# Kernel optimization log

Measured on AMD Instinct MI355X. Metric: run time of the kernel, lower is better.

## Reference

```python
import jax, jax.numpy as jnp
import numpy as np
from jax import lax

K = 3          # dcn kernel size
KK = K * K     # 9 taps
PAD = 1


def _conv(x, w, b, pad):
    y = lax.conv_general_dilated(
        x, w, window_strides=(1, 1), padding=[(pad, pad), (pad, pad)],
        dimension_numbers=("NCHW", "OIHW", "NCHW"))
    return y + b[None, :, None, None]


def _bilinear_gather(x, py, px):
    """Zero-padded bilinear sampling.
    x: [B,C,Hin,Win]; py,px: [B,KK,H,W] float sample coords.
    returns [B,C,KK,H,W]."""
    B, C, Hin, Win = x.shape
    y0 = jnp.floor(py)
    x0 = jnp.floor(px)
    ly = py - y0   # frac weights
    lx = px - x0
    xf = x.reshape(B, C, Hin * Win)

    def corner(yc, xc, w):
        valid = (yc >= 0) & (yc <= Hin - 1) & (xc >= 0) & (xc <= Win - 1)
        yi = jnp.clip(yc, 0, Hin - 1).astype(jnp.int32)
        xi = jnp.clip(xc, 0, Win - 1).astype(jnp.int32)
        idx = yi * Win + xi                              # [B,KK,H,W]
        vals = jax.vmap(lambda f, i: jnp.take(f, i, axis=1))(xf, idx)  # [B,C,KK,H,W]
        return vals * (w * valid.astype(x.dtype))[:, None]

    out = corner(y0,     x0,     (1 - ly) * (1 - lx))
    out = out + corner(y0,     x0 + 1, (1 - ly) * lx)
    out = out + corner(y0 + 1, x0,     ly * (1 - lx))
    out = out + corner(y0 + 1, x0 + 1, ly * lx)
    return out


def _forward(x, conv1_w, conv1_b, off_w, off_b, dcn_w, dcn_b):
    # features: Conv2d(1,3,3,s1,p1) + ReLU + MaxPool(3,2)
    h = jax.nn.relu(_conv(x, conv1_w, conv1_b, pad=1))
    h = lax.reduce_window(h, -jnp.inf, lax.max,
                          window_dimensions=(1, 1, 3, 3),
                          window_strides=(1, 1, 2, 2), padding="VALID")
    B, C, H, W = h.shape

    # DCNv2: conv_offset_mask -> (dy, dx, sigmoid mask)
    om = _conv(h, off_w, off_b, pad=PAD)          # [B, 3*KK, H, W]
    dy = om[:, :KK]
    dx = om[:, KK:2 * KK]
    mask = jax.nn.sigmoid(om[:, 2 * KK:])         # [B, KK, H, W]

    # base sampling grid (stride 1, pad 1, dilation 1)
    ky = (jnp.arange(KK) // K).astype(h.dtype)    # kernel row of each tap
    kx = (jnp.arange(KK) % K).astype(h.dtype)
    hh = jnp.arange(H, dtype=h.dtype)
    ww = jnp.arange(W, dtype=h.dtype)
    py = hh[None, None, :, None] - PAD + ky[None, :, None, None] + dy
    px = ww[None, None, None, :] - PAD + kx[None, :, None, None] + dx

    sampled = _bilinear_gather(h, py, px)          # [B,C,KK,H,W]
    sampled = sampled * mask[:, None]              # modulation
    out = jnp.einsum("bckhw,ock->bohw", sampled,
                     dcn_w.reshape(dcn_w.shape[0], C, KK))
    return out + dcn_b[None, :, None, None]


def setup_inputs() -> dict:
    key = jax.random.key(0)
    ks = jax.random.split(key, 7)
    x = jax.random.normal(ks[0], (32, 1, 512, 512), dtype=jnp.float32)
    conv1_w = jax.random.normal(ks[1], (3, 1, 3, 3), dtype=jnp.float32) * 0.5
    conv1_b = jnp.zeros((3,), dtype=jnp.float32)
    # offset/mask conv: 3*KK = 27 output channels; small init so offsets are modest
    off_w = jax.random.normal(ks[2], (3 * KK, 3, 3, 3), dtype=jnp.float32) * 0.01
    off_b = jax.random.normal(ks[3], (3 * KK,), dtype=jnp.float32) * 0.01
    dcn_w = jax.random.normal(ks[4], (3, 3, 3, 3), dtype=jnp.float32) * 0.1
    dcn_b = jnp.zeros((3,), dtype=jnp.float32)
    return {"x": x, "conv1_w": conv1_w, "conv1_b": conv1_b,
            "off_w": off_w, "off_b": off_b, "dcn_w": dcn_w, "dcn_b": dcn_b}


def reference(x, conv1_w, conv1_b, off_w, off_b, dcn_w, dcn_b):
    return _forward(x, conv1_w, conv1_b, off_w, off_b, dcn_w, dcn_b)
```

## Files before the change

kernel.cpp:

```cpp
#include <hip/hip_runtime.h>
#include <hip/hip_fp16.h>
#include <math.h>

#define B_  32
#define H0  512
#define W0  512
#define Hh  255
#define Wh  255
#define HP  259

typedef __attribute__((ext_vector_type(8))) _Float16 f16x8;
typedef __attribute__((ext_vector_type(4))) float    f32x4;
typedef __attribute__((ext_vector_type(4))) unsigned int u32x4;

static __device__ __forceinline__ __half2 u2h2(unsigned int u) {
    __half2 h; __builtin_memcpy(&h, &u, 4); return h;
}
static __device__ __forceinline__ unsigned int h2u(__half2 h) {
    unsigned int u; __builtin_memcpy(&u, &h, 4); return u;
}

__global__ __launch_bounds__(256) void conv_pool_kernel(
    const float* __restrict__ x,
    const float* __restrict__ w,
    const float* __restrict__ bias,
    uint2* __restrict__ hp)
{
    const int b = blockIdx.z;
    const int tx = threadIdx.x, ty = threadIdx.y;
    const int tid = ty * 16 + tx;

    if (blockIdx.y == 16) {
        uint2* hpb = hp + b * (HP * HP);
        const int gid = blockIdx.x * 256 + tid;
        if (gid < 2072) {
            int r, c;
            if (gid < 1036) {
                int rr = gid / 259; c = gid - rr * 259;
                r = rr + (rr >= 2 ? 255 : 0);
            } else {
                int u = gid - 1036;
                int cc = u / 259; r = u - cc * 259;
                c = cc + (cc >= 2 ? 255 : 0);
            }
            hpb[r * HP + c] = make_uint2(0u, 0u);
        }
        return;
    }

    __shared__ float sx[35][36];
    __shared__ float sc[33 * 100];
    const int i0 = blockIdx.y * 16;
    const int j0 = blockIdx.x * 16;

    const float* xb = x + b * (H0 * W0);
    for (int t = tid; t < 35 * 35; t += 256) {
        int r = t / 35, c = t - r * 35;
        int gr = 2 * i0 - 1 + r;
        int gc = 2 * j0 - 1 + c;
        float v = 0.f;
        if ((unsigned)gr < (unsigned)H0 && (unsigned)gc < (unsigned)W0) v = xb[gr * W0 + gc];
        sx[r][c] = v;
    }
    __syncthreads();

    float w0[9], w1[9], w2[9];
#pragma unroll
    for (int t = 0; t < 9; ++t) { w0[t] = w[t]; w1[t] = w[9 + t]; w2[t] = w[18 + t]; }
    const float b0 = bias[0], b1 = bias[1], b2 = bias[2];

    for (int t = tid; t < 33 * 33; t += 256) {
        int r = t / 33, c = t - r * 33;
        float s0 = b0, s1 = b1, s2 = b2;
#pragma unroll
        for (int ky = 0; ky < 3; ++ky) {
#pragma unroll
            for (int kx = 0; kx < 3; ++kx) {
                float v = sx[r + ky][c + kx];
                s0 = fmaf(w0[ky * 3 + kx], v, s0);
                s1 = fmaf(w1[ky * 3 + kx], v, s1);
                s2 = fmaf(w2[ky * 3 + kx], v, s2);
            }
        }
        float* p = &sc[r * 100 + c * 3];
        p[0] = s0; p[1] = s1; p[2] = s2;
    }
    __syncthreads();

    const int i = i0 + ty, j = j0 + tx;
    if (i >= Hh || j >= Wh) return;

    const float* r0 = &sc[(2 * ty + 0) * 100 + (2 * tx) * 3];
    const float* r1 = &sc[(2 * ty + 1) * 100 + (2 * tx) * 3];
    const float* r2 = &sc[(2 * ty + 2) * 100 + (2 * tx) * 3];
#define MAX3_(a, bq, cq) fmaxf(fmaxf((a), (bq)), (cq))
    float m0 = MAX3_(MAX3_(r0[0], r0[3], r0[6]), MAX3_(r1[0], r1[3], r1[6]), MAX3_(r2[0], r2[3], r2[6]));
    float m1 = MAX3_(MAX3_(r0[1], r0[4], r0[7]), MAX3_(r1[1], r1[4], r1[7]), MAX3_(r2[1], r2[4], r2[7]));
    float m2 = MAX3_(MAX3_(r0[2], r0[5], r0[8]), MAX3_(r1[2], r1[5], r1[8]), MAX3_(r2[2], r2[5], r2[8]));
    m0 = fmaxf(m0, 0.f); m1 = fmaxf(m1, 0.f); m2 = fmaxf(m2, 0.f);

    uint2 v;
    v.x = h2u(__floats2half2_rn(m0, m1));
    v.y = (unsigned int)__half_as_ushort(__float2half_rn(m2));
    hp[(b * HP + i + 2) * HP + (j + 2)] = v;
}

__global__ __launch_bounds__(256, 5) void dcn_kernel(
    const uint2* __restrict__ hp,
    const float* __restrict__ off_w,
    const float* __restrict__ off_b,
    const float* __restrict__ dcn_w,
    const float* __restrict__ dcn_b,
    float* __restrict__ out)
{
    __shared__ __align__(16) char smem[18432];

    const int y   = blockIdx.x;
    const int b   = blockIdx.y;
    const int tid = threadIdx.x;
    const int x   = tid;

    const uint2* hb = hp + b * (HP * HP);

    {
        unsigned short* Bm = (unsigned short*)(smem + 16384);
        for (int idx = tid; idx < 1024; idx += 256) {
            int n = idx >> 5, k = idx & 31;
            float v = 0.f;
            if (n < 27) { if (k < 27) v = off_w[n * 27 + k]; else if (k == 27) v = off_b[n]; }
            Bm[n * 32 + k] = __half_as_ushort(__float2half_rn(v));
        }
    }

    unsigned int L[9], Hv[9];
#pragma unroll
    for (int ky = 0; ky < 3; ++ky) {
        const unsigned int rbase = (unsigned int)(y + 1 + ky) * HP + (unsigned int)(x + 1);
        u32x4 r01;
        __builtin_memcpy(&r01, hb + rbase, 16);
        uint2 r2 = hb[rbase + 2];
        L[ky * 3 + 0]  = r01.x;  Hv[ky * 3 + 0] = r01.y;
        L[ky * 3 + 1]  = r01.z;  Hv[ky * 3 + 1] = r01.w;
        L[ky * 3 + 2]  = r2.x;   Hv[ky * 3 + 2] = r2.y;
    }

    {
        unsigned int T[16];
        T[0]  = (L[0] & 0xFFFFu) | (L[1] << 16);
        T[1]  = (L[2] & 0xFFFFu) | (L[3] << 16);
        T[2]  = (L[4] & 0xFFFFu) | (L[5] << 16);
        T[3]  = (L[6] & 0xFFFFu) | (L[7] << 16);
        T[4]  = (L[8] & 0xFFFFu) | (L[0] & 0xFFFF0000u);
        T[5]  = (L[1] >> 16) | (L[2] & 0xFFFF0000u);
        T[6]  = (L[3] >> 16) | (L[4] & 0xFFFF0000u);
        T[7]  = (L[5] >> 16) | (L[6] & 0xFFFF0000u);
        T[8]  = (L[7] >> 16) | (L[8] & 0xFFFF0000u);
        T[9]  = (Hv[0] & 0xFFFFu) | (Hv[1] << 16);
        T[10] = (Hv[2] & 0xFFFFu) | (Hv[3] << 16);
        T[11] = (Hv[4] & 0xFFFFu) | (Hv[5] << 16);
        T[12] = (Hv[6] & 0xFFFFu) | (Hv[7] << 16);
        T[13] = (Hv[8] & 0xFFFFu) | 0x3C000000u;
        T[14] = 0u;
        T[15] = 0u;
#pragma unroll
        for (int c4 = 0; c4 < 4; ++c4) {
            u32x4 v = { T[c4 * 4 + 0], T[c4 * 4 + 1], T[c4 * 4 + 2], T[c4 * 4 + 3] };
            *(u32x4*)(smem + (c4 * 256 + tid) * 16) = v;
        }
    }
    __syncthreads();

    {
        const int wave = tid >> 6, lane = tid & 63;
        const int lrow = lane & 15, lchunk = lane >> 4;
        const _Float16* As = (const _Float16*)smem;
        const _Float16* Bs = (const _Float16*)(smem + 16384);

        f16x8 afr[4];
#pragma unroll
        for (int m = 0; m < 4; ++m)
            afr[m] = *(const f16x8*)(As + (lchunk * 256 + wave * 64 + m * 16 + lrow) * 8);
        f16x8 bfr[2];
#pragma unroll
        for (int nt = 0; nt < 2; ++nt)
            bfr[nt] = *(const f16x8*)(Bs + ((nt * 16 + lrow) * 32 + lchunk * 8));

        f32x4 acc[4][2];
#pragma unroll
        for (int m = 0; m < 4; ++m)
#pragma unroll
            for (int nt = 0; nt < 2; ++nt) {
                f32x4 z = {0.f, 0.f, 0.f, 0.f};
                acc[m][nt] = __builtin_amdgcn_mfma_f32_16x16x32_f16(bfr[nt], afr[m], z, 0, 0, 0);
            }
        __syncthreads();

#pragma unroll
        for (int m = 0; m < 4; ++m)
#pragma unroll
            for (int nt = 0; nt < 2; ++nt) {
                const int n0  = nt * 16 + lchunk * 4;
                const int pxw = wave * 64 + m * 16 + lrow;
                unsigned int p0 = h2u(__floats2half2_rn(acc[m][nt][0], acc[m][nt][1]));
                unsigned int p1 = h2u(__floats2half2_rn(acc[m][nt][2], acc[m][nt][3]));
                unsigned int* q = (unsigned int*)(smem + pxw * 68 + n0 * 2);
                q[0] = p0;
                q[1] = p1;
            }
    }
    __syncthreads();

    unsigned int o2[14];
    {
        const unsigned int* omp = (const unsigned int*)(smem + x * 68);
#pragma unroll
        for (int j = 0; j < 14; ++j) o2[j] = omp[j];
    }
#define OM_(n) (((n) & 1) ? __high2float(u2h2(o2[(n) >> 1])) : __low2float(u2h2(o2[(n) >> 1])))

    float outv0 = dcn_b[0], outv1 = dcn_b[1], outv2 = dcn_b[2];
    const float yf = (float)y, xf = (float)x;

#pragma unroll
    for (int k = 0; k < 9; ++k) {
        const float dy  = OM_(k);
        const float dxx = OM_(9 + k);
        const float zm  = OM_(18 + k);
        const float msk = __builtin_amdgcn_rcpf(1.f + __expf(-zm));

        const float py = fminf(fmaxf(yf + (float)(k / 3 - 1) + dy,  -2.f), 255.f);
        const float px = fminf(fmaxf(xf + (float)(k % 3 - 1) + dxx, -2.f), 255.f);

        const float y0f = floorf(py), x0f = floorf(px);
        const float ly = py - y0f, lx = px - x0f;
        const int iy = (int)y0f + 2;
        const int ix = (int)x0f + 2;

        const unsigned int idx = (unsigned int)iy * HP + (unsigned int)ix;
        u32x4 ua, ub;
        __builtin_memcpy(&ua, hb + idx, 16);
        __builtin_memcpy(&ub, hb + idx + HP, 16);

        const float my1 = ly * msk;
        const float my0 = msk - my1;
        const float lx1 = 1.f - lx;
        const float w00 = my0 * lx1, w01 = my0 * lx;
        const float w10 = my1 * lx1, w11 = my1 * lx;

        const __half2 W00 = __float2half2_rn(w00);
        const __half2 W01 = __float2half2_rn(w01);
        const __half2 W10 = __float2half2_rn(w10);
        const __half2 W11 = __float2half2_rn(w11);
        __half2 sA = __hmul2(W00, u2h2(ua.x));
        sA = __hfma2(W01, u2h2(ua.z), sA);
        sA = __hfma2(W10, u2h2(ub.x), sA);
        sA = __hfma2(W11, u2h2(ub.z), sA);
        __half2 sB = __hmul2(W00, u2h2(ua.y));
        sB = __hfma2(W01, u2h2(ua.w), sB);
        sB = __hfma2(W10, u2h2(ub.y), sB);
        sB = __hfma2(W11, u2h2(ub.w), sB);
        const float s0 = __low2float(sA);
        const float s1 = __high2float(sA);
        const float s2 = __low2float(sB);

        outv0 = fmaf(dcn_w[0 * 27 + 0 * 9 + k], s0, outv0);
        outv0 = fmaf(dcn_w[0 * 27 + 1 * 9 + k], s1, outv0);
        outv0 = fmaf(dcn_w[0 * 27 + 2 * 9 + k], s2, outv0);
        outv1 = fmaf(dcn_w[1 * 27 + 0 * 9 + k], s0, outv1);
        outv1 = fmaf(dcn_w[1 * 27 + 1 * 9 + k], s1, outv1);
        outv1 = fmaf(dcn_w[1 * 27 + 2 * 9 + k], s2, outv1);
        outv2 = fmaf(dcn_w[2 * 27 + 0 * 9 + k], s0, outv2);
        outv2 = fmaf(dcn_w[2 * 27 + 1 * 9 + k], s1, outv2);
        outv2 = fmaf(dcn_w[2 * 27 + 2 * 9 + k], s2, outv2);
    }

    if (x < Wh) {
        const int hwsz = Hh * Wh;
        const int o = (b * 3) * hwsz + y * Wh + x;
        out[o]            = outv0;
        out[o + hwsz]     = outv1;
        out[o + 2 * hwsz] = outv2;
    }
}

extern "C" void kernel_launch(void* const* d_in, const int* in_sizes, int n_in,
                              void* d_out, int out_size, void* d_ws, size_t ws_size,
                              hipStream_t stream) {
    const float* x       = (const float*)d_in[0];
    const float* conv1_w = (const float*)d_in[1];
    const float* conv1_b = (const float*)d_in[2];
    const float* off_w   = (const float*)d_in[3];
    const float* off_b   = (const float*)d_in[4];
    const float* dcn_w   = (const float*)d_in[5];
    const float* dcn_b   = (const float*)d_in[6];
    float* out = (float*)d_out;
    uint2* hp  = (uint2*)d_ws;

    conv_pool_kernel<<<dim3(16, 17, B_), dim3(16, 16), 0, stream>>>(x, conv1_w, conv1_b, hp);
    dcn_kernel<<<dim3(Hh, B_), 256, 0, stream>>>(hp, off_w, off_b, dcn_w, dcn_b, out);
}
```

Baseline: 67.12 us.

## Move final DCN channel reduction onto MFMA via shared-memory staging

Each thread keeps its nine fp16 bilinear-sampled tap vectors, stores them to LDS, and a wave runs two 16x16x32 f16 MFMAs per 16-pixel tile against dcn weights and bias packed into LDS. This replaces the 81 scalar fp32 FMAs per pixel. It also drops the barrier between the offset-MFMA output writes and their reads, relying on each wave reading only rows it wrote itself. The tradeoff is extra LDS traffic, a larger shared buffer, fp16 weights in the final reduction, and output stores done by only 3 of 16 lanes per group.

```diff
diff --git a/kernel.cpp b/kernel.cpp
--- a/kernel.cpp
+++ b/kernel.cpp
@@ -8,6 +8,10 @@
 #define Hh  255
 #define Wh  255
 #define HP  259
+
+#define OFF_BOFF 20480
+#define OFF_B1D  22528
+#define OFF_B2D  23552
 
 typedef __attribute__((ext_vector_type(8))) _Float16 f16x8;
 typedef __attribute__((ext_vector_type(4))) float    f32x4;
@@ -113,22 +117,40 @@
     const float* __restrict__ dcn_b,
     float* __restrict__ out)
 {
-    __shared__ __align__(16) char smem[18432];
-
-    const int y   = blockIdx.x;
-    const int b   = blockIdx.y;
-    const int tid = threadIdx.x;
-    const int x   = tid;
+    __shared__ __align__(16) char smem[24576];
+
+    const int y    = blockIdx.x;
+    const int b    = blockIdx.y;
+    const int tid  = threadIdx.x;
+    const int x    = tid;
+    const int wave = tid >> 6, lane = tid & 63;
+    const int lrow = lane & 15, lchunk = lane >> 4;
 
     const uint2* hb = hp + b * (HP * HP);
 
     {
-        unsigned short* Bm = (unsigned short*)(smem + 16384);
+        unsigned short* Bm = (unsigned short*)(smem + OFF_BOFF);
         for (int idx = tid; idx < 1024; idx += 256) {
             int n = idx >> 5, k = idx & 31;
             float v = 0.f;
             if (n < 27) { if (k < 27) v = off_w[n * 27 + k]; else if (k == 27) v = off_b[n]; }
             Bm[n * 32 + k] = __half_as_ushort(__float2half_rn(v));
+        }
+    }
+    {
+        unsigned short* B1 = (unsigned short*)(smem + OFF_B1D);
+        unsigned short* B2 = (unsigned short*)(smem + OFF_B2D);
+        for (int idx = tid; idx < 512; idx += 256) {
+            int n = idx >> 5, k = idx & 31;
+            float v1 = 0.f, v2 = 0.f;
+            if (n < 3) {
+                int tap = k >> 2, c = k & 3;
+                if (c < 3) v1 = dcn_w[n * 27 + c * 9 + tap];
+                if (k < 3) v2 = dcn_w[n * 27 + k * 9 + 8];
+                else if (k == 4) v2 = dcn_b[n];
+            }
+            B1[n * 32 + k] = __half_as_ushort(__float2half_rn(v1));
+            B2[n * 32 + k] = __half_as_ushort(__float2half_rn(v2));
         }
     }
 
@@ -171,10 +193,8 @@
     __syncthreads();
 
     {
-        const int wave = tid >> 6, lane = tid & 63;
-        const int lrow = lane & 15, lchunk = lane >> 4;
         const _Float16* As = (const _Float16*)smem;
-        const _Float16* Bs = (const _Float16*)(smem + 16384);
+        const _Float16* Bs = (const _Float16*)(smem + OFF_BOFF);
 
         f16x8 afr[4];
 #pragma unroll
@@ -208,7 +228,6 @@
                 q[1] = p1;
             }
     }
-    __syncthreads();
 
     unsigned int o2[14];
     {
@@ -218,7 +237,7 @@
     }
 #define OM_(n) (((n) & 1) ? __high2float(u2h2(o2[(n) >> 1])) : __low2float(u2h2(o2[(n) >> 1])))
 
-    float outv0 = dcn_b[0], outv1 = dcn_b[1], outv2 = dcn_b[2];
+    unsigned int sAv[9], sBv[9];
     const float yf = (float)y, xf = (float)x;
 
 #pragma unroll
@@ -259,27 +278,52 @@
         sB = __hfma2(W01, u2h2(ua.w), sB);
         sB = __hfma2(W10, u2h2(ub.y), sB);
         sB = __hfma2(W11, u2h2(ub.w), sB);
-        const float s0 = __low2float(sA);
-        const float s1 = __high2float(sA);
-        const float s2 = __low2float(sB);
-
-        outv0 = fmaf(dcn_w[0 * 27 + 0 * 9 + k], s0, outv0);
-        outv0 = fmaf(dcn_w[0 * 27 + 1 * 9 + k], s1, outv0);
-        outv0 = fmaf(dcn_w[0 * 27 + 2 * 9 + k], s2, outv0);
-        outv1 = fmaf(dcn_w[1 * 27 + 0 * 9 + k], s0, outv1);
-        outv1 = fmaf(dcn_w[1 * 27 + 1 * 9 + k], s1, outv1);
-        outv1 = fmaf(dcn_w[1 * 27 + 2 * 9 + k], s2, outv1);
-        outv2 = fmaf(dcn_w[2 * 27 + 0 * 9 + k], s0, outv2);
-        outv2 = fmaf(dcn_w[2 * 27 + 1 * 9 + k], s1, outv2);
-        outv2 = fmaf(dcn_w[2 * 27 + 2 * 9 + k], s2, outv2);
-    }
-
-    if (x < Wh) {
-        const int hwsz = Hh * Wh;
-        const int o = (b * 3) * hwsz + y * Wh + x;
-        out[o]            = outv0;
-        out[o + hwsz]     = outv1;
-        out[o + 2 * hwsz] = outv2;
+        sAv[k] = h2u(sA);
+        sBv[k] = h2u(sB);
+    }
+
+    __syncthreads();
+
+    {
+        char* a2 = smem + tid * 80;
+#pragma unroll
+        for (int g = 0; g < 4; ++g) {
+            u32x4 v = { sAv[2 * g], sBv[2 * g], sAv[2 * g + 1], sBv[2 * g + 1] };
+            *(u32x4*)(a2 + g * 16) = v;
+        }
+        u32x4 v4 = { sAv[8], sBv[8], 0x00003C00u, 0u };
+        *(u32x4*)(a2 + 64) = v4;
+    }
+
+    {
+        const _Float16* B1 = (const _Float16*)(smem + OFF_B1D);
+        const _Float16* B2 = (const _Float16*)(smem + OFF_B2D);
+        const f16x8 bd1 = *(const f16x8*)(B1 + (lrow * 32 + lchunk * 8));
+        const f16x8 bd2 = *(const f16x8*)(B2 + (lrow * 32 + lchunk * 8));
+
+        const int n  = lrow;
+        const int hw = Hh * Wh;
+        float* ob = out + (b * 3 + n) * hw + y * Wh;
+
+#pragma unroll
+        for (int m = 0; m < 4; ++m) {
+            const int pxb = (wave * 64 + m * 16 + lrow) * 80;
+            f16x8 a2a = *(const f16x8*)((const _Float16*)(smem + pxb + lchunk * 16));
+            f16x8 a2b = *(const f16x8*)((const _Float16*)(smem + pxb + 64 + lchunk * 16));
+            f32x4 z = {0.f, 0.f, 0.f, 0.f};
+            f32x4 acc = __builtin_amdgcn_mfma_f32_16x16x32_f16(a2a, bd1, z, 0, 0, 0);
+            acc = __builtin_amdgcn_mfma_f32_16x16x32_f16(a2b, bd2, acc, 0, 0, 0);
+
+            if (n < 3) {
+                const int xb = wave * 64 + m * 16 + lchunk * 4;
+                float* po = ob + xb;
+                if (xb < 252) {
+                    po[0] = acc[0]; po[1] = acc[1]; po[2] = acc[2]; po[3] = acc[3];
+                } else {
+                    po[0] = acc[0]; po[1] = acc[1]; po[2] = acc[2];
+                }
+            }
+        }
     }
 }
 
```

Result: slower. 75.85 us (+13.0%).
